# Performance work log

Hardware: AMD Instinct MI355X
Metric: run time of the kernel (lower is better)

The kernel has to match this reference:

```python
import jax, jax.numpy as jnp
import numpy as np

# Config matching GConv(in_channels=64, out_channels=64, kernel_type=1,
#                       is_first=False, rot_1x1_in=False, stride=1, padding=1, dilation=1)
KERNEL_TYPE = 1
NUM_KERNEL = 9      # taps per sparse kernel
KERNEL_ROT = 4      # number of rotations
STEP = 8 // KERNEL_ROT
STRIDE, PAD, DIL = 1, 1, 1
CIN, COUT = 64, 64

# Ring of the 8 neighbor offsets (dy, dx) in 45-degree steps around the center.
RING = [(-1, -1), (-1, 0), (-1, 1), (0, 1), (1, 1), (1, 0), (1, -1), (0, -1)]

def tap_offsets(kernel_type, rot8):
    """Tap positions of the sparse 3x3 kernel, rotated by rot8 * 45 degrees."""
    if kernel_type == 1:      # full 3x3: center + 8 ring taps
        ring_ids = list(range(8))
    elif kernel_type == 0:    # skeleton: center + 4-cross
        ring_ids = [0, 2, 4, 6]
    else:                     # bar: center + opposite pair
        ring_ids = [0, 4]
    return [(0, 0)] + [RING[(i + rot8) % 8] for i in ring_ids]


def sparse_spatial_conv(x, w, offs):
    """x: [N, C, H, W], w: [O, C, T], offs: T tap offsets.
    Each tap contributes its own output-channel group (no tap summation):
    returns [N, T*O, Ho, Wo] with tap-major channel ordering (matches torch.cat)."""
    N, C, H, W = x.shape
    Ho = (H + 2 * PAD - (DIL * 2 + 1)) // STRIDE + 1
    Wo = (W + 2 * PAD - (DIL * 2 + 1)) // STRIDE + 1
    xp = jnp.pad(x, ((0, 0), (0, 0), (PAD, PAD), (PAD, PAD)))
    shifts = []
    for dy, dx in offs:
        sh, sw = (dy + 1) * DIL, (dx + 1) * DIL
        shifts.append(xp[:, :, sh:sh + (Ho - 1) * STRIDE + 1:STRIDE,
                             sw:sw + (Wo - 1) * STRIDE + 1:STRIDE])
    xs = jnp.stack(shifts, axis=0)               # [T, N, C, Ho, Wo]
    out = jnp.einsum('tnchw,oct->tnohw', xs, w)  # per-tap 1x1 conv at shifted pos
    Tt = out.shape[0]
    return out.transpose(1, 0, 2, 3, 4).reshape(N, Tt * w.shape[0], Ho, Wo)


def setup_inputs() -> dict:
    key = jax.random.key(0)
    k1, k2 = jax.random.split(key)
    x_tensor = jax.random.normal(k1, (8, CIN, KERNEL_ROT, 64, 64), dtype=jnp.float32)
    weight = jax.random.normal(k2, (COUT, CIN, KERNEL_ROT, NUM_KERNEL), dtype=jnp.float32) * 0.05
    return {"x_tensor": x_tensor, "weight": weight}


def reference(x_tensor, weight):
    N, Cin, R, H, W = x_tensor.shape
    # cat rotation dim into channels (rot-major): [N, R*Cin, H, W]
    x_cat = x_tensor.transpose(0, 2, 1, 3, 4).reshape(N, R * Cin, H, W)
    O = weight.shape[0]
    rot_out = []
    for rot in range(KERNEL_ROT):
        # rotated weight gather: cat weight[:, :, (idx - rot) % R, :] over idx along dim=1
        idxs = (np.arange(R) - rot) % R
        w_rot = weight[:, :, idxs, :]                    # [O, Cin, R, T]
        w_rot = w_rot.transpose(0, 2, 1, 3).reshape(O, R * Cin, NUM_KERNEL)
        offs = tap_offsets(KERNEL_TYPE, STEP * rot)
        rot_out.append(sparse_spatial_conv(x_cat, w_rot, offs))  # [N, T*O, Ho, Wo]
    return jnp.stack(rot_out, axis=2)  # [N, T*O, R, Ho, Wo]
```

## Files before the change

### kernel.cpp

```cpp
#include <hip/hip_runtime.h>
#include <stdint.h>

using short8 = __attribute__((ext_vector_type(8))) short;
using f32x4  = __attribute__((ext_vector_type(4))) float;

__device__ __forceinline__ unsigned short f2bf(float f) {
    unsigned int u = __float_as_uint(f);
    unsigned int r = (u + 0x7fffu + ((u >> 16) & 1u)) >> 16;
    return (unsigned short)r;
}

__global__ __launch_bounds__(256) void k_prep(const float* __restrict__ x,
                                              const float* __restrict__ wgt,
                                              unsigned short* __restrict__ xt,
                                              unsigned short* __restrict__ ball) {
    __shared__ unsigned short sm[256][72];
    int b = blockIdx.x;
    int tid = threadIdx.x;
    if (b < 512) {
        int n = b >> 6; int h = b & 63;
        int c = tid >> 2, r = tid & 3; int k = r * 64 + c;
        const float* src = x + ((((size_t)n * 64 + c) * 4 + r) * 64 + h) * 64;
#pragma unroll
        for (int i = 0; i < 64; i += 4) {
            float4 v = *(const float4*)(src + i);
            sm[k][i + 0] = f2bf(v.x); sm[k][i + 1] = f2bf(v.y);
            sm[k][i + 2] = f2bf(v.z); sm[k][i + 3] = f2bf(v.w);
        }
        __syncthreads();
        int w = tid & 63, kg = tid >> 6;
        unsigned short* dst = xt + ((size_t)(n * 66 + (h + 1)) * 64 + w) * 256;
        int key = (w + 1) & 7;
#pragma unroll
        for (int cc = 0; cc < 8; cc++) {
            int s = kg * 8 + cc; int sp = s ^ key;
            short8 v;
#pragma unroll
            for (int e = 0; e < 8; e++) v[e] = (short)sm[s * 8 + e][w];
            *(short8*)(dst + sp * 8) = v;
        }
    } else if (b < 640) {
        int idx = (b - 512) * 256 + tid;
        int n = idx >> 12; int rr = (idx >> 11) & 1; int cpos = idx & 2047;
        f32x4 z = {0.f, 0.f, 0.f, 0.f};
        *(f32x4*)((char*)xt + (size_t)(n * 66 + (rr ? 65 : 0)) * 32768 + cpos * 16) = z;
    } else {
        int idx = (b - 640) * 256 + tid;
        int k = idx & 255; int col = (idx >> 8) & 255; int j = idx >> 16;
        int rot = col >> 6, o = col & 63;
        int r = k >> 6, c = k & 63;
        int t = (j == 0) ? 0 : (1 + ((j - 1 - 2 * rot) & 7));
        float v = wgt[((o * 64 + c) * 4 + ((r - rot) & 3)) * 9 + t];
        ball[idx] = f2bf(v);
    }
}

__global__ __launch_bounds__(512) void k_main(const unsigned short* __restrict__ xt,
                                              const unsigned short* __restrict__ ball,
                                              float* __restrict__ out) {
    extern __shared__ char lds[];
    int blk = blockIdx.x; int n = blk >> 5; int h0 = (blk & 31) * 2;
    int tid = threadIdx.x;

    const char* xbase = (const char*)xt;
#pragma unroll
    for (int i = 0; i < 16; i++) {
        int chunk = tid + i * 512;
        int r4 = chunk >> 11; int cin = chunk & 2047;
        const char* src = xbase + (size_t)(n * 66 + h0 + r4) * 32768 + cin * 16;
        char* dst = lds + r4 * 33792 + 512 + cin * 16;
        __builtin_amdgcn_global_load_lds(
            (const __attribute__((address_space(1))) unsigned int*)src,
            (__attribute__((address_space(3))) unsigned int*)dst, 16, 0, 0);
    }
    if (tid < 256) {
        int r4 = tid >> 6; int sp = (tid >> 5) & 1; int cc = tid & 31;
        f32x4 z = {0.f, 0.f, 0.f, 0.f};
        *(f32x4*)(lds + r4 * 33792 + (sp ? 65 * 512 : 0) + cc * 16) = z;
    }
    __syncthreads();

    int wv = tid >> 6; int l = tid & 63; int l15 = l & 15; int l4 = l >> 4;
    int rot = wv >> 1;
    const char* bb = (const char*)ball;

    for (int j = 0; j < 9; j++) {
        int dy = ((0x1A901 >> (2 * j)) & 3) - 1;
        int dx = ((0x01A91 >> (2 * j)) & 3) - 1;
        int t = (j == 0) ? 0 : (1 + ((j - 1 - 2 * rot) & 7));

        short8 Bf[2][8];
#pragma unroll
        for (int ct = 0; ct < 2; ct++) {
            int col = wv * 32 + ct * 16 + l15;
            const char* bp = bb + j * 131072 + col * 512 + l4 * 16;
#pragma unroll
            for (int ks = 0; ks < 8; ks++) Bf[ct][ks] = *(const short8*)(bp + ks * 64);
        }

#pragma unroll 1
        for (int mtp = 0; mtp < 4; mtp++) {
            short8 Af[2][8];
#pragma unroll
            for (int m2 = 0; m2 < 2; m2++) {
                int mt = mtp * 2 + m2;
                int pixel = mt * 16 + l15;
                int r4 = (pixel >> 6) + dy + 1;
                int ws = (pixel & 63) + dx + 1;
                const char* ap = lds + (r4 * 66 + ws) * 512;
                int key = ws & 7;
#pragma unroll
                for (int ks = 0; ks < 8; ks++) {
                    int s = ks * 4 + l4;
                    Af[m2][ks] = *(const short8*)(ap + ((s ^ key) << 4));
                }
            }
            f32x4 acc[2][2];
#pragma unroll
            for (int a = 0; a < 2; a++)
#pragma unroll
                for (int b2 = 0; b2 < 2; b2++) acc[a][b2] = (f32x4){0.f, 0.f, 0.f, 0.f};
#pragma unroll
            for (int ks = 0; ks < 8; ks++)
#pragma unroll
                for (int ct = 0; ct < 2; ct++)
#pragma unroll
                    for (int m2 = 0; m2 < 2; m2++)
                        acc[ct][m2] = __builtin_amdgcn_mfma_f32_16x16x32_bf16(
                            Af[m2][ks], Bf[ct][ks], acc[ct][m2], 0, 0, 0);
#pragma unroll
            for (int ct = 0; ct < 2; ct++) {
                int o = (wv & 1) * 32 + ct * 16 + l15;
#pragma unroll
                for (int m2 = 0; m2 < 2; m2++) {
                    int mt = mtp * 2 + m2;
                    int pb = mt * 16 + 4 * l4;
                    int h = h0 + (mt >> 2);
                    int wb = pb & 63;
                    int idx = (((n * 576 + t * 64 + o) * 4 + rot) * 64 + h) * 64 + wb;
                    *(f32x4*)(out + idx) = acc[ct][m2];
                }
            }
        }
    }
}

__global__ __launch_bounds__(256) void k_naive(const float* __restrict__ x,
                                               const float* __restrict__ wgt,
                                               float* __restrict__ out) {
    int idx = blockIdx.x * 256 + threadIdx.x;
    if (idx >= 75497472) return;
    int w = idx & 63, h = (idx >> 6) & 63, rot = (idx >> 12) & 3;
    int chn = idx >> 14; int ch = chn % 576; int n = chn / 576;
    int t = ch >> 6, o = ch & 63;
    int dy = 0, dx = 0;
    if (t > 0) {
        int ri = (t - 1 + 2 * rot) & 7;
        dy = ((27200 >> (2 * ri)) & 3) - 1;
        dx = ((1700 >> (2 * ri)) & 3) - 1;
    }
    int hh = h + dy, ww = w + dx;
    float acc = 0.f;
    if (hh >= 0 && hh < 64 && ww >= 0 && ww < 64) {
        for (int r = 0; r < 4; r++) {
            int rr = (r - rot) & 3;
            for (int c = 0; c < 64; c++)
                acc += x[(((n * 64 + c) * 4 + r) * 64 + hh) * 64 + ww] *
                       wgt[((o * 64 + c) * 4 + rr) * 9 + t];
        }
    }
    out[idx] = acc;
}

extern "C" void kernel_launch(void* const* d_in, const int* in_sizes, int n_in,
                              void* d_out, int out_size, void* d_ws, size_t ws_size,
                              hipStream_t stream) {
    const float* x = (const float*)d_in[0];
    const float* wgt = (const float*)d_in[1];
    float* out = (float*)d_out;
    const size_t XT_BYTES = (size_t)8 * 66 * 64 * 256 * 2;
    const size_t NEED = XT_BYTES + (size_t)9 * 256 * 256 * 2;
    if (ws_size < NEED) {
        k_naive<<<(75497472 + 255) / 256, 256, 0, stream>>>(x, wgt, out);
        return;
    }
    unsigned short* xt = (unsigned short*)d_ws;
    unsigned short* ball = (unsigned short*)((char*)d_ws + XT_BYTES);
    k_prep<<<2944, 256, 0, stream>>>(x, wgt, xt, ball);
    k_main<<<256, 512, 135168, stream>>>(xt, ball, out);
}
```

Measured before the change: 90.54 us.

## Stage MFMA accumulators through LDS for contiguous row-wise output stores

Each tap now keeps all four m-tile pairs' accumulators live in registers, then transposes them through a per-wave swizzled LDS slice. Each 64-lane store then writes two full 128-float output rows instead of scattered 16-byte pieces. The aim is better write coalescing on the output, which dominates the memory traffic. The cost is more registers (64 accumulator floats per lane), extra LDS (dynamic size raised to 151552 bytes), and intra-wave LDS round trips guarded by schedule barriers.

```diff
diff --git a/kernel.cpp b/kernel.cpp
--- a/kernel.cpp
+++ b/kernel.cpp
@@ -83,6 +83,8 @@
     int wv = tid >> 6; int l = tid & 63; int l15 = l & 15; int l4 = l >> 4;
     int rot = wv >> 1;
     const char* bb = (const char*)ball;
+    char* slice = lds + 135168 + wv * 2048;
+    const int KEY[4] = {0, 5, 2, 7};
 
     for (int j = 0; j < 9; j++) {
         int dy = ((0x1A901 >> (2 * j)) & 3) - 1;
@@ -98,7 +100,15 @@
             for (int ks = 0; ks < 8; ks++) Bf[ct][ks] = *(const short8*)(bp + ks * 64);
         }
 
-#pragma unroll 1
+        f32x4 acc[4][2][2];
+#pragma unroll
+        for (int a = 0; a < 4; a++)
+#pragma unroll
+            for (int b2 = 0; b2 < 2; b2++)
+#pragma unroll
+                for (int c2 = 0; c2 < 2; c2++) acc[a][b2][c2] = (f32x4){0.f, 0.f, 0.f, 0.f};
+
+#pragma unroll
         for (int mtp = 0; mtp < 4; mtp++) {
             short8 Af[2][8];
 #pragma unroll
@@ -115,32 +125,42 @@
                     Af[m2][ks] = *(const short8*)(ap + ((s ^ key) << 4));
                 }
             }
-            f32x4 acc[2][2];
-#pragma unroll
-            for (int a = 0; a < 2; a++)
-#pragma unroll
-                for (int b2 = 0; b2 < 2; b2++) acc[a][b2] = (f32x4){0.f, 0.f, 0.f, 0.f};
 #pragma unroll
             for (int ks = 0; ks < 8; ks++)
 #pragma unroll
                 for (int ct = 0; ct < 2; ct++)
 #pragma unroll
                     for (int m2 = 0; m2 < 2; m2++)
-                        acc[ct][m2] = __builtin_amdgcn_mfma_f32_16x16x32_bf16(
-                            Af[m2][ks], Bf[ct][ks], acc[ct][m2], 0, 0, 0);
-#pragma unroll
-            for (int ct = 0; ct < 2; ct++) {
-                int o = (wv & 1) * 32 + ct * 16 + l15;
-#pragma unroll
-                for (int m2 = 0; m2 < 2; m2++) {
-                    int mt = mtp * 2 + m2;
-                    int pb = mt * 16 + 4 * l4;
-                    int h = h0 + (mt >> 2);
-                    int wb = pb & 63;
-                    int idx = (((n * 576 + t * 64 + o) * 4 + rot) * 64 + h) * 64 + wb;
-                    *(f32x4*)(out + idx) = acc[ct][m2];
-                }
+                        acc[mtp][ct][m2] = __builtin_amdgcn_mfma_f32_16x16x32_bf16(
+                            Af[m2][ks], Bf[ct][ks], acc[mtp][ct][m2], 0, 0, 0);
+        }
+
+        size_t outb = ((size_t)(n * 576 + t * 64) * 4 + rot) * 4096 + (size_t)h0 * 64;
+#pragma unroll
+        for (int r = 0; r < 8; r++) {
+            int ct = r >> 2; int q = r & 3;
+            if ((l15 >> 2) == q) {
+                int orow = l15 & 3;
+#pragma unroll
+                for (int mtp = 0; mtp < 4; mtp++)
+#pragma unroll
+                    for (int m2 = 0; m2 < 2; m2++) {
+                        int chunk = (mtp * 2 + m2) * 4 + l4;
+                        *(f32x4*)(slice + orow * 512 + ((chunk ^ KEY[orow]) << 4)) =
+                            acc[mtp][ct][m2];
+                    }
             }
+            __builtin_amdgcn_sched_barrier(0);
+            int o8 = ct * 16 + q * 4;
+#pragma unroll
+            for (int i = 0; i < 2; i++) {
+                int o_loc = o8 + 2 * i + (l >> 5);
+                int orow = o_loc & 3;
+                f32x4 v = *(const f32x4*)(slice + orow * 512 + (((l & 31) ^ KEY[orow]) << 4));
+                int o = (wv & 1) * 32 + o_loc;
+                *(f32x4*)(out + outb + (size_t)o * 16384 + (l & 31) * 4) = v;
+            }
+            __builtin_amdgcn_sched_barrier(0);
         }
     }
 }
@@ -187,5 +207,5 @@
     unsigned short* xt = (unsigned short*)d_ws;
     unsigned short* ball = (unsigned short*)((char*)d_ws + XT_BYTES);
     k_prep<<<2944, 256, 0, stream>>>(x, wgt, xt, ball);
-    k_main<<<256, 512, 135168, stream>>>(xt, ball, out);
-}
+    k_main<<<256, 512, 151552, stream>>>(xt, ball, out);
+}
```

After: 104.0 us. 1.15x slower.

## Repartition main kernel waves by rotation and row to cover all output channels

Applied to the files above, without the earlier changes.

Each of the 8 waves now owns one rotation and one of the two output rows and computes all 64 output channels, instead of half the channels across both rows. Each wave loads B fragments for 64 columns (double the register footprint) and one row of A tiles, which halves A-fragment LDS reads per MFMA and drops the double-buffered m2 loop. The tap loop is no longer unrolled, and the inner 4-tile loop is fully unrolled with four accumulators. The higher VGPR use for Bf could hurt occupancy or cause spills.

```diff
diff --git a/kernel.cpp b/kernel.cpp
--- a/kernel.cpp
+++ b/kernel.cpp
@@ -81,66 +81,53 @@
     __syncthreads();
 
     int wv = tid >> 6; int l = tid & 63; int l15 = l & 15; int l4 = l >> 4;
-    int rot = wv >> 1;
+    int rot = wv & 3; int mhalf = wv >> 2;
+    int h = h0 + mhalf;
     const char* bb = (const char*)ball;
 
+#pragma unroll 1
     for (int j = 0; j < 9; j++) {
         int dy = ((0x1A901 >> (2 * j)) & 3) - 1;
         int dx = ((0x01A91 >> (2 * j)) & 3) - 1;
         int t = (j == 0) ? 0 : (1 + ((j - 1 - 2 * rot) & 7));
+        int r4 = mhalf + dy + 1;
+        const char* arow = lds + r4 * 33792;
 
-        short8 Bf[2][8];
+        short8 Bf[4][8];
 #pragma unroll
-        for (int ct = 0; ct < 2; ct++) {
-            int col = wv * 32 + ct * 16 + l15;
-            const char* bp = bb + j * 131072 + col * 512 + l4 * 16;
+        for (int ct = 0; ct < 4; ct++) {
+            const char* bp = bb + j * 131072 + (rot * 64 + ct * 16 + l15) * 512 + l4 * 16;
 #pragma unroll
             for (int ks = 0; ks < 8; ks++) Bf[ct][ks] = *(const short8*)(bp + ks * 64);
         }
 
-#pragma unroll 1
-        for (int mtp = 0; mtp < 4; mtp++) {
-            short8 Af[2][8];
+        size_t outb = ((size_t)(n * 576 + t * 64) * 4 + rot) * 4096 + (size_t)h * 64;
 #pragma unroll
-            for (int m2 = 0; m2 < 2; m2++) {
-                int mt = mtp * 2 + m2;
-                int pixel = mt * 16 + l15;
-                int r4 = (pixel >> 6) + dy + 1;
-                int ws = (pixel & 63) + dx + 1;
-                const char* ap = lds + (r4 * 66 + ws) * 512;
-                int key = ws & 7;
+        for (int mt = 0; mt < 4; mt++) {
+            int ws = mt * 16 + l15 + dx + 1;
+            const char* ap = arow + ws * 512;
+            int key = ws & 7;
+            short8 Af[8];
 #pragma unroll
-                for (int ks = 0; ks < 8; ks++) {
-                    int s = ks * 4 + l4;
-                    Af[m2][ks] = *(const short8*)(ap + ((s ^ key) << 4));
-                }
+            for (int ks = 0; ks < 8; ks++) {
+                int s = ks * 4 + l4;
+                Af[ks] = *(const short8*)(ap + ((s ^ key) << 4));
             }
-            f32x4 acc[2][2];
+            f32x4 a0 = {0.f,0.f,0.f,0.f}, a1 = {0.f,0.f,0.f,0.f};
+            f32x4 a2 = {0.f,0.f,0.f,0.f}, a3 = {0.f,0.f,0.f,0.f};
 #pragma unroll
-            for (int a = 0; a < 2; a++)
-#pragma unroll
-                for (int b2 = 0; b2 < 2; b2++) acc[a][b2] = (f32x4){0.f, 0.f, 0.f, 0.f};
-#pragma unroll
-            for (int ks = 0; ks < 8; ks++)
-#pragma unroll
-                for (int ct = 0; ct < 2; ct++)
-#pragma unroll
-                    for (int m2 = 0; m2 < 2; m2++)
-                        acc[ct][m2] = __builtin_amdgcn_mfma_f32_16x16x32_bf16(
-                            Af[m2][ks], Bf[ct][ks], acc[ct][m2], 0, 0, 0);
-#pragma unroll
-            for (int ct = 0; ct < 2; ct++) {
-                int o = (wv & 1) * 32 + ct * 16 + l15;
-#pragma unroll
-                for (int m2 = 0; m2 < 2; m2++) {
-                    int mt = mtp * 2 + m2;
-                    int pb = mt * 16 + 4 * l4;
-                    int h = h0 + (mt >> 2);
-                    int wb = pb & 63;
-                    int idx = (((n * 576 + t * 64 + o) * 4 + rot) * 64 + h) * 64 + wb;
-                    *(f32x4*)(out + idx) = acc[ct][m2];
-                }
+            for (int ks = 0; ks < 8; ks++) {
+                a0 = __builtin_amdgcn_mfma_f32_16x16x32_bf16(Af[ks], Bf[0][ks], a0, 0, 0, 0);
+                a1 = __builtin_amdgcn_mfma_f32_16x16x32_bf16(Af[ks], Bf[1][ks], a1, 0, 0, 0);
+                a2 = __builtin_amdgcn_mfma_f32_16x16x32_bf16(Af[ks], Bf[2][ks], a2, 0, 0, 0);
+                a3 = __builtin_amdgcn_mfma_f32_16x16x32_bf16(Af[ks], Bf[3][ks], a3, 0, 0, 0);
             }
+            int wb = mt * 16 + 4 * l4;
+            float* ob = out + outb + wb;
+            *(f32x4*)(ob + (size_t)(0 * 16 + l15) * 16384) = a0;
+            *(f32x4*)(ob + (size_t)(1 * 16 + l15) * 16384) = a1;
+            *(f32x4*)(ob + (size_t)(2 * 16 + l15) * 16384) = a2;
+            *(f32x4*)(ob + (size_t)(3 * 16 + l15) * 16384) = a3;
         }
     }
 }
```

Measured after the change: 123.4 us. 36.3% more time.
